# Performance work log

Measured on AMD Instinct MI355X. Metric: run time of the kernel, lower is better.

## Reference

```python
import jax, jax.numpy as jnp
import numpy as np

EPS = 1e-5


def _bn(h, gamma, beta):
    # BatchNorm1d in training mode: batch statistics over node dim
    mu = h.mean(axis=0)
    var = h.var(axis=0)
    return gamma * (h - mu) * jax.lax.rsqrt(var + EPS) + beta


def _rgcn_layer(x, src, dst, etype, W, Wloop, b, n_dst):
    # Relation-specific gather-transform-scatter (DGL RelGraphConv, sum agg,
    # self-loop + bias, no regularizer).
    x_src = x[src]                                   # [E, in] gather
    num_rels = W.shape[0]
    m = jnp.zeros((x_src.shape[0], W.shape[2]), x.dtype)
    for r in range(num_rels):                        # small fixed relation count
        m = m + jnp.where((etype == r)[:, None], x_src @ W[r], 0.0)
    agg = jax.ops.segment_sum(m, dst, num_segments=n_dst)  # scatter-add to dst
    # DGL block convention: dst nodes are the prefix of src nodes
    return agg + x[:n_dst] @ Wloop + b


def setup_inputs() -> dict:
    key = jax.random.key(0)
    ks = jax.random.split(key, 16)
    N_SRC, N_DST0, N_DST1 = 200000, 50000, 10000
    E0, E1, R, H, C = 800000, 160000, 5, 256, 153
    s = 1.0 / np.sqrt(H)
    inp = {
        "x": jax.random.normal(ks[0], (N_SRC, H), jnp.float32),
        "src0": jax.random.randint(ks[1], (E0,), 0, N_SRC, jnp.int32),
        "dst0": jax.random.randint(ks[2], (E0,), 0, N_DST0, jnp.int32),
        "etype0": jax.random.randint(ks[3], (E0,), 0, R, jnp.int32),
        "src1": jax.random.randint(ks[4], (E1,), 0, N_DST0, jnp.int32),
        "dst1": jax.random.randint(ks[5], (E1,), 0, N_DST1, jnp.int32),
        "etype1": jax.random.randint(ks[6], (E1,), 0, R, jnp.int32),
        "n_dst0": N_DST0,
        "n_dst1": N_DST1,
        "W0": jax.random.normal(ks[7], (R, H, H), jnp.float32) * s,
        "Wl0": jax.random.normal(ks[8], (H, H), jnp.float32) * s,
        "b0": jnp.zeros((H,), jnp.float32),
        "g0": jnp.ones((H,), jnp.float32),
        "be0": jnp.zeros((H,), jnp.float32),
        "W1": jax.random.normal(ks[9], (R, H, H), jnp.float32) * s,
        "Wl1": jax.random.normal(ks[10], (H, H), jnp.float32) * s,
        "b1": jnp.zeros((H,), jnp.float32),
        "g1": jnp.ones((H,), jnp.float32),
        "be1": jnp.zeros((H,), jnp.float32),
        "Wm1": jax.random.normal(ks[11], (H, H), jnp.float32) * s,
        "bm1": jnp.zeros((H,), jnp.float32),
        "gm": jnp.ones((H,), jnp.float32),
        "bem": jnp.zeros((H,), jnp.float32),
        "Wm2": jax.random.normal(ks[12], (H, C), jnp.float32) * s,
        "bm2": jnp.zeros((C,), jnp.float32),
    }
    return inp


def reference(x, src0, dst0, etype0, src1, dst1, etype1, n_dst0, n_dst1,
              W0, Wl0, b0, g0, be0, W1, Wl1, b1, g1, be1,
              Wm1, bm1, gm, bem, Wm2, bm2):
    # layer 0
    h = _rgcn_layer(x, src0, dst0, etype0, W0, Wl0, b0, n_dst0)
    h = jax.nn.elu(_bn(h, g0, be0))
    # layer 1
    h = _rgcn_layer(h, src1, dst1, etype1, W1, Wl1, b1, n_dst1)
    h = jax.nn.elu(_bn(h, g1, be1))
    # MLP head (dropout is identity in eval)
    h = jax.nn.relu(_bn(h @ Wm1 + bm1, gm, bem))
    return h @ Wm2 + bm2
```

## Files before the change

kernel.cpp:

```cpp
#include <hip/hip_runtime.h>
#include <hip/hip_bf16.h>


#define HD   256
#define EPS  1e-5f
#define NREL 5
#define ND0  50000
#define ND1  10000

typedef unsigned short ushort_t;
using f32x4  = __attribute__((ext_vector_type(4))) float;
using short8 = __attribute__((ext_vector_type(8))) short;

__device__ __forceinline__ ushort_t f2b(float f) {
    union { float f; unsigned u; } x; x.f = f;
    unsigned r = x.u + 0x7FFF + ((x.u >> 16) & 1);
    return (ushort_t)(r >> 16);
}
__device__ __forceinline__ float b2f(ushort_t h) {
    union { unsigned u; float f; } x; x.u = ((unsigned)h) << 16;
    return x.f;
}

#define GLOAD_LDS16(gp, lp)                                                     \
    __builtin_amdgcn_global_load_lds(                                           \
        (const __attribute__((address_space(1))) unsigned int*)(gp),            \
        (__attribute__((address_space(3))) unsigned int*)(lp), 16, 0, 0)

struct WconvArgs {
    const float* src[14];
    ushort_t*    dst[14];
    int          N[14];
};
__global__ void wconv_all_kernel(WconvArgs a) {
    int mat = blockIdx.x >> 8;
    int id = (blockIdx.x & 255) * 256 + threadIdx.x;
    int n = id >> 8, k = id & 255;
    int N = a.N[mat];
    float v = (n < N) ? a.src[mat][(size_t)k * N + n] : 0.f;
    a.dst[mat][id] = f2b(v);
}

__global__ void xconv_kernel(const float* __restrict__ x, ushort_t* __restrict__ xb,
                             int n4) {
    int id = blockIdx.x * 256 + threadIdx.x;
    if (id >= n4) return;
    float4 v = ((const float4*)x)[id];
    ushort4 o; o.x = f2b(v.x); o.y = f2b(v.y); o.z = f2b(v.z); o.w = f2b(v.w);
    ((ushort4*)xb)[id] = o;
}

__global__ void count2_kernel(const int* __restrict__ d0, const int* __restrict__ e0, int E0,
                              const int* __restrict__ d1, const int* __restrict__ e1, int E1,
                              int* __restrict__ cnt, int* __restrict__ pos) {
    int e = blockIdx.x * 256 + threadIdx.x;
    if (e < E0) {
        pos[e] = atomicAdd(&cnt[e0[e] * ND0 + d0[e]], 1);
    } else if (e < E0 + E1) {
        int i = e - E0;
        pos[e] = atomicAdd(&cnt[NREL * ND0 + e1[i] * ND1 + d1[i]], 1);
    }
}

__global__ void scan_block_kernel(const int* __restrict__ in, int* __restrict__ out,
                                  int* __restrict__ bsum, int nb) {
    __shared__ int ts[256];
    int tid = threadIdx.x;
    int base = blockIdx.x * 1024 + tid * 4;
    int v0 = (base + 0 < nb) ? in[base + 0] : 0;
    int v1 = (base + 1 < nb) ? in[base + 1] : 0;
    int v2 = (base + 2 < nb) ? in[base + 2] : 0;
    int v3 = (base + 3 < nb) ? in[base + 3] : 0;
    int tsum = v0 + v1 + v2 + v3;
    ts[tid] = tsum;
    __syncthreads();
    for (int d = 1; d < 256; d <<= 1) {
        int t = (tid >= d) ? ts[tid - d] : 0;
        __syncthreads();
        ts[tid] += t;
        __syncthreads();
    }
    int excl = ts[tid] - tsum;
    if (base + 0 < nb) out[base + 0] = excl;
    if (base + 1 < nb) out[base + 1] = excl + v0;
    if (base + 2 < nb) out[base + 2] = excl + v0 + v1;
    if (base + 3 < nb) out[base + 3] = excl + v0 + v1 + v2;
    if (tid == 255 && bsum) bsum[blockIdx.x] = ts[255];
}

__global__ void scan_add_kernel(int* __restrict__ out, const int* __restrict__ bsum, int nb) {
    int i = blockIdx.x * 256 + threadIdx.x;
    if (i < nb) out[i] += bsum[i >> 10];
}

__global__ void fill2_kernel(const int* __restrict__ s0, const int* __restrict__ d0,
                             const int* __restrict__ e0, int E0,
                             const int* __restrict__ s1, const int* __restrict__ d1,
                             const int* __restrict__ e1, int E1,
                             const int* __restrict__ pos, const int* __restrict__ off,
                             int* __restrict__ ssrc) {
    int e = blockIdx.x * 256 + threadIdx.x;
    if (e < E0) {
        ssrc[off[e0[e] * ND0 + d0[e]] + pos[e]] = s0[e];
    } else if (e < E0 + E1) {
        int i = e - E0;
        ssrc[off[NREL * ND0 + e1[i] * ND1 + d1[i]] + pos[e]] = s1[i];
    }
}

__global__ void gather_kernel(const ushort_t* __restrict__ feat, const int* __restrict__ ssrc,
                              const int* __restrict__ cnt, const int* __restrict__ off,
                              int nbuckets, ushort_t* __restrict__ out,
                              const float* __restrict__ sc, const float* __restrict__ sh) {
    int wave = (blockIdx.x * 256 + threadIdx.x) >> 6;
    int lane = threadIdx.x & 63;
    if (wave >= nbuckets) return;
    int deg = cnt[wave], s = off[wave];
    float4 scv = {0, 0, 0, 0}, shv = {0, 0, 0, 0};
    if (sc) { scv = ((const float4*)sc)[lane]; shv = ((const float4*)sh)[lane]; }
    float a0 = 0, a1 = 0, a2 = 0, a3 = 0;
    if (sc) {
        for (int j = 0; j < deg; j++) {
            ushort4 v = ((const ushort4*)(feat + (size_t)ssrc[s + j] * HD))[lane];
            float f0 = fmaf(b2f(v.x), scv.x, shv.x);
            float f1 = fmaf(b2f(v.y), scv.y, shv.y);
            float f2 = fmaf(b2f(v.z), scv.z, shv.z);
            float f3 = fmaf(b2f(v.w), scv.w, shv.w);
            a0 += f0 > 0.f ? f0 : expm1f(f0);
            a1 += f1 > 0.f ? f1 : expm1f(f1);
            a2 += f2 > 0.f ? f2 : expm1f(f2);
            a3 += f3 > 0.f ? f3 : expm1f(f3);
        }
    } else {
        int j = 0;
        for (; j + 2 <= deg; j += 2) {
            int r0 = ssrc[s + j], r1 = ssrc[s + j + 1];
            ushort4 v0 = ((const ushort4*)(feat + (size_t)r0 * HD))[lane];
            ushort4 v1 = ((const ushort4*)(feat + (size_t)r1 * HD))[lane];
            a0 += b2f(v0.x) + b2f(v1.x); a1 += b2f(v0.y) + b2f(v1.y);
            a2 += b2f(v0.z) + b2f(v1.z); a3 += b2f(v0.w) + b2f(v1.w);
        }
        if (j < deg) {
            ushort4 v = ((const ushort4*)(feat + (size_t)ssrc[s + j] * HD))[lane];
            a0 += b2f(v.x); a1 += b2f(v.y); a2 += b2f(v.z); a3 += b2f(v.w);
        }
    }
    ushort4 o; o.x = f2b(a0); o.y = f2b(a1); o.z = f2b(a2); o.w = f2b(a3);
    ((ushort4*)(out + (size_t)wave * HD))[lane] = o;
}

__global__ void bnprep_kernel(const float* __restrict__ sums, const float* __restrict__ g,
                              const float* __restrict__ be, float invM,
                              float* __restrict__ sc, float* __restrict__ sh) {
    int c = threadIdx.x;
    float mu = sums[c] * invM;
    float var = sums[HD + c] * invM - mu * mu;
    float s = g[c] * rsqrtf(var + EPS);
    sc[c] = s; sh[c] = be[c] - mu * s;
}

__global__ void bnact_kernel(const ushort_t* __restrict__ in, ushort_t* __restrict__ out,
                             const float* __restrict__ sc, const float* __restrict__ sh,
                             int act, int n64) {
    int id = blockIdx.x * 256 + threadIdx.x;
    if (id >= n64) return;
    int c4 = id & 63;
    ushort4 v = ((const ushort4*)in)[id];
    float4 scv = ((const float4*)sc)[c4];
    float4 shv = ((const float4*)sh)[c4];
    float f0 = fmaf(b2f(v.x), scv.x, shv.x);
    float f1 = fmaf(b2f(v.y), scv.y, shv.y);
    float f2 = fmaf(b2f(v.z), scv.z, shv.z);
    float f3 = fmaf(b2f(v.w), scv.w, shv.w);
    if (act == 2) {
        f0 = fmaxf(f0, 0.f); f1 = fmaxf(f1, 0.f);
        f2 = fmaxf(f2, 0.f); f3 = fmaxf(f3, 0.f);
    } else {
        f0 = f0 > 0.f ? f0 : expm1f(f0);
        f1 = f1 > 0.f ? f1 : expm1f(f1);
        f2 = f2 > 0.f ? f2 : expm1f(f2);
        f3 = f3 > 0.f ? f3 : expm1f(f3);
    }
    ushort4 o; o.x = f2b(f0); o.y = f2b(f1); o.z = f2b(f2); o.w = f2b(f3);
    ((ushort4*)out)[id] = o;
}

struct Seg {
    const ushort_t* A;
    const ushort_t* B;
};
struct GemmArgs {
    Seg seg[6];
    int nseg;
    const float* bias;
    float* stats;
    ushort_t* Cb;
    float* Cf;
    int M, N;
};

__launch_bounds__(256, 2)
__global__ void gemm_ring_kernel(GemmArgs g) {
    __shared__ __align__(1024) ushort_t As[4][4096];
    __shared__ __align__(1024) ushort_t Bs[4][4096];
    int tid = threadIdx.x;
    int w = tid >> 6, lane = tid & 63;
    int rq = lane >> 4, ci = lane & 15;
    int wm = (w >> 1) * 64, wn = (w & 1) * 64;
    int wmf = wm >> 4, wnf = wn >> 4;
    int bm = blockIdx.y * 128, bn = blockIdx.x * 128;
    f32x4 acc[4][4] = {};
    int NT = (g.nseg * HD) >> 5;

    auto stage = [&](int b, int t) {
        int k = t << 5;
        int si = k >> 8, kl = k & 255;
        const ushort_t* Ap = g.seg[si].A;
        const ushort_t* Bp = g.seg[si].B;
        int ft = w * 2;
        GLOAD_LDS16(Ap + (size_t)(bm + ft * 16 + ci) * HD + kl + rq * 8,
                    &As[b][ft * 512 + lane * 8]);
        GLOAD_LDS16(Ap + (size_t)(bm + (ft + 1) * 16 + ci) * HD + kl + rq * 8,
                    &As[b][(ft + 1) * 512 + lane * 8]);
        GLOAD_LDS16(Bp + (size_t)(bn + ft * 16 + ci) * HD + kl + rq * 8,
                    &Bs[b][ft * 512 + lane * 8]);
        GLOAD_LDS16(Bp + (size_t)(bn + (ft + 1) * 16 + ci) * HD + kl + rq * 8,
                    &Bs[b][(ft + 1) * 512 + lane * 8]);
    };

    stage(0, 0);
    if (NT > 1) stage(1, 1);
    if (NT > 2) stage(2, 2);
    for (int t = 0; t < NT; t++) {
        int buf = t & 3;
        int rem = NT - t;
        if (rem >= 3)      asm volatile("s_waitcnt vmcnt(8)" ::: "memory");
        else if (rem == 2) asm volatile("s_waitcnt vmcnt(4)" ::: "memory");
        else               asm volatile("s_waitcnt vmcnt(0)" ::: "memory");
        __builtin_amdgcn_s_barrier();
        __builtin_amdgcn_sched_barrier(0);
        if (t + 3 < NT) stage((t + 3) & 3, t + 3);
        short8 a[4], b[4];
#pragma unroll
        for (int ni = 0; ni < 4; ni++)
            b[ni] = *(const short8*)&Bs[buf][(wnf + ni) * 512 + lane * 8];
#pragma unroll
        for (int mi = 0; mi < 4; mi++)
            a[mi] = *(const short8*)&As[buf][(wmf + mi) * 512 + lane * 8];
#pragma unroll
        for (int mi = 0; mi < 4; mi++)
#pragma unroll
            for (int ni = 0; ni < 4; ni++)
                acc[mi][ni] = __builtin_amdgcn_mfma_f32_16x16x32_bf16(
                    a[mi], b[ni], acc[mi][ni], 0, 0, 0);
    }

#pragma unroll
    for (int ni = 0; ni < 4; ni++) {
        int col = bn + wn + ni * 16 + ci;
        float bv = (col < g.N) ? g.bias[col] : 0.f;
#pragma unroll
        for (int mi = 0; mi < 4; mi++)
#pragma unroll
            for (int reg = 0; reg < 4; reg++) acc[mi][ni][reg] += bv;
    }
    if (g.stats) {
#pragma unroll
        for (int ni = 0; ni < 4; ni++) {
            float s = 0.f, s2 = 0.f;
#pragma unroll
            for (int mi = 0; mi < 4; mi++)
#pragma unroll
                for (int reg = 0; reg < 4; reg++) {
                    int row = bm + wm + mi * 16 + rq * 4 + reg;
                    if (row < g.M) { float v = acc[mi][ni][reg]; s += v; s2 += v * v; }
                }
            s  += __shfl_xor(s, 16);  s  += __shfl_xor(s, 32);
            s2 += __shfl_xor(s2, 16); s2 += __shfl_xor(s2, 32);
            if (rq == 0) {
                int col = bn + wn + ni * 16 + ci;
                atomicAdd(&g.stats[col], s);
                atomicAdd(&g.stats[HD + col], s2);
            }
        }
    }
#pragma unroll
    for (int mi = 0; mi < 4; mi++)
#pragma unroll
        for (int ni = 0; ni < 4; ni++)
#pragma unroll
            for (int reg = 0; reg < 4; reg++) {
                int row = bm + wm + mi * 16 + rq * 4 + reg;
                int col = bn + wn + ni * 16 + ci;
                if (row < g.M && col < g.N) {
                    float v = acc[mi][ni][reg];
                    if (g.Cb) g.Cb[(size_t)row * HD + col] = f2b(v);
                    else      g.Cf[(size_t)row * g.N + col] = v;
                }
            }
}

extern "C" void kernel_launch(void* const* d_in, const int* in_sizes, int n_in,
                              void* d_out, int out_size, void* d_ws, size_t ws_size,
                              hipStream_t stream) {
    const float* x   = (const float*)d_in[0];
    const int* src0  = (const int*)d_in[1];
    const int* dst0  = (const int*)d_in[2];
    const int* et0   = (const int*)d_in[3];
    const int* src1  = (const int*)d_in[4];
    const int* dst1  = (const int*)d_in[5];
    const int* et1   = (const int*)d_in[6];
    const float* W0  = (const float*)d_in[9];
    const float* Wl0 = (const float*)d_in[10];
    const float* b0  = (const float*)d_in[11];
    const float* g0  = (const float*)d_in[12];
    const float* be0 = (const float*)d_in[13];
    const float* W1  = (const float*)d_in[14];
    const float* Wl1 = (const float*)d_in[15];
    const float* b1  = (const float*)d_in[16];
    const float* g1  = (const float*)d_in[17];
    const float* be1 = (const float*)d_in[18];
    const float* Wm1 = (const float*)d_in[19];
    const float* bm1 = (const float*)d_in[20];
    const float* gm  = (const float*)d_in[21];
    const float* bem = (const float*)d_in[22];
    const float* Wm2 = (const float*)d_in[23];
    const float* bm2 = (const float*)d_in[24];

    const int E0 = in_sizes[1];
    const int E1 = in_sizes[4];
    const int NOUT = in_sizes[24];
    const int NSRC = in_sizes[0] / HD;
    const int NBKT = NREL * ND0 + NREL * ND1;

    char* p = (char*)d_ws;
    ushort_t* Wt = (ushort_t*)p;  p += (size_t)14 * 65536 * 2;
    float* st    = (float*)p;     p += 1536 * 4;
    float* bnp   = (float*)p;     p += 6 * 256 * 4;
    int* cnt     = (int*)p;       p += (size_t)NBKT * 4;
    int* off     = (int*)p;       p += (size_t)NBKT * 4;
    int* bsum    = (int*)p;       p += 1024 * 4;
    int* pos     = (int*)p;       p += (size_t)(E0 + E1) * 4;
    int* ssrc    = (int*)p;       p += (size_t)(E0 + E1) * 4;
    ushort_t* xb  = (ushort_t*)p; p += (size_t)NSRC * HD * 2;
    ushort_t* S0  = (ushort_t*)p; p += (size_t)(NREL * ND0 + 512) * HD * 2;
    ushort_t* S1  = (ushort_t*)p; p += (size_t)(NREL * ND1 + 512) * HD * 2;
    ushort_t* h0b = (ushort_t*)p; p += (size_t)(ND0 + 512) * HD * 2;
    ushort_t* h1b = (ushort_t*)p; p += (size_t)(ND1 + 512) * HD * 2;
    ushort_t* mb  = (ushort_t*)p; p += (size_t)(ND1 + 512) * HD * 2;
    ushort_t* h0a = (ushort_t*)p; p += (size_t)(ND1 + 512) * HD * 2;
    ushort_t* h1a = (ushort_t*)p; p += (size_t)(ND1 + 512) * HD * 2;
    ushort_t* ma  = (ushort_t*)p; p += (size_t)(ND1 + 512) * HD * 2;

    float* st0 = st, *st1 = st + 512, *stm = st + 1024;
    float* sc0 = bnp, *sh0 = bnp + 256, *sc1 = bnp + 512, *sh1 = bnp + 768;
    float* scm = bnp + 1024, *shm = bnp + 1280;

    ushort_t* W0t  = Wt;
    ushort_t* Wl0t = Wt + 5 * 65536;
    ushort_t* W1t  = Wt + 6 * 65536;
    ushort_t* Wl1t = Wt + 11 * 65536;
    ushort_t* Wm1t = Wt + 12 * 65536;
    ushort_t* Wm2t = Wt + 13 * 65536;

    {
        WconvArgs wa;
        for (int r = 0; r < NREL; r++) { wa.src[r] = W0 + (size_t)r * 65536; wa.dst[r] = W0t + (size_t)r * 65536; wa.N[r] = 256; }
        wa.src[5] = Wl0; wa.dst[5] = Wl0t; wa.N[5] = 256;
        for (int r = 0; r < NREL; r++) { wa.src[6 + r] = W1 + (size_t)r * 65536; wa.dst[6 + r] = W1t + (size_t)r * 65536; wa.N[6 + r] = 256; }
        wa.src[11] = Wl1; wa.dst[11] = Wl1t; wa.N[11] = 256;
        wa.src[12] = Wm1; wa.dst[12] = Wm1t; wa.N[12] = 256;
        wa.src[13] = Wm2; wa.dst[13] = Wm2t; wa.N[13] = NOUT;
        wconv_all_kernel<<<14 * 256, 256, 0, stream>>>(wa);
    }
    xconv_kernel<<<(NSRC * 64 + 255) / 256, 256, 0, stream>>>(x, xb, NSRC * 64);
    hipMemsetAsync(st, 0, 1536 * sizeof(float), stream);
    hipMemsetAsync(cnt, 0, (size_t)NBKT * sizeof(int), stream);

    int ET = E0 + E1;
    count2_kernel<<<(ET + 255) / 256, 256, 0, stream>>>(dst0, et0, E0, dst1, et1, E1, cnt, pos);
    int nsb = (NBKT + 1023) / 1024;
    scan_block_kernel<<<nsb, 256, 0, stream>>>(cnt, off, bsum, NBKT);
    scan_block_kernel<<<1, 256, 0, stream>>>(bsum, bsum, nullptr, nsb);
    scan_add_kernel<<<(NBKT + 255) / 256, 256, 0, stream>>>(off, bsum, NBKT);
    fill2_kernel<<<(ET + 255) / 256, 256, 0, stream>>>(src0, dst0, et0, E0, src1, dst1, et1, E1, pos, off, ssrc);

    gather_kernel<<<(NREL * ND0 * 64) / 256, 256, 0, stream>>>(
        xb, ssrc, cnt, off, NREL * ND0, S0, nullptr, nullptr);
    {
        GemmArgs ga = {};
        for (int s = 0; s < NREL; s++)
            ga.seg[s] = { S0 + (size_t)s * ND0 * HD, W0t + (size_t)s * 65536 };
        ga.seg[5] = { xb, Wl0t };
        ga.nseg = 6; ga.bias = b0; ga.stats = st0;
        ga.Cb = h0b; ga.Cf = nullptr; ga.M = ND0; ga.N = HD;
        gemm_ring_kernel<<<dim3(2, (ND0 + 127) / 128), 256, 0, stream>>>(ga);
    }
    bnprep_kernel<<<1, 256, 0, stream>>>(st0, g0, be0, 1.f / ND0, sc0, sh0);

    bnact_kernel<<<((ND1 + 512) * 64 + 255) / 256, 256, 0, stream>>>(
        h0b, h0a, sc0, sh0, 1, (ND1 + 512) * 64);
    gather_kernel<<<(NREL * ND1 * 64) / 256, 256, 0, stream>>>(
        h0b, ssrc, cnt + NREL * ND0, off + NREL * ND0, NREL * ND1, S1, sc0, sh0);
    {
        GemmArgs ga = {};
        for (int s = 0; s < NREL; s++)
            ga.seg[s] = { S1 + (size_t)s * ND1 * HD, W1t + (size_t)s * 65536 };
        ga.seg[5] = { h0a, Wl1t };
        ga.nseg = 6; ga.bias = b1; ga.stats = st1;
        ga.Cb = h1b; ga.Cf = nullptr; ga.M = ND1; ga.N = HD;
        gemm_ring_kernel<<<dim3(2, (ND1 + 127) / 128), 256, 0, stream>>>(ga);
    }
    bnprep_kernel<<<1, 256, 0, stream>>>(st1, g1, be1, 1.f / ND1, sc1, sh1);

    bnact_kernel<<<((ND1 + 512) * 64 + 255) / 256, 256, 0, stream>>>(
        h1b, h1a, sc1, sh1, 1, (ND1 + 512) * 64);
    {
        GemmArgs ga = {};
        ga.seg[0] = { h1a, Wm1t };
        ga.nseg = 1; ga.bias = bm1; ga.stats = stm;
        ga.Cb = mb; ga.Cf = nullptr; ga.M = ND1; ga.N = HD;
        gemm_ring_kernel<<<dim3(2, (ND1 + 127) / 128), 256, 0, stream>>>(ga);
    }
    bnprep_kernel<<<1, 256, 0, stream>>>(stm, gm, bem, 1.f / ND1, scm, shm);
    bnact_kernel<<<((ND1 + 512) * 64 + 255) / 256, 256, 0, stream>>>(
        mb, ma, scm, shm, 2, (ND1 + 512) * 64);
    {
        GemmArgs ga = {};
        ga.seg[0] = { ma, Wm2t };
        ga.nseg = 1; ga.bias = bm2; ga.stats = nullptr;
        ga.Cb = nullptr; ga.Cf = (float*)d_out; ga.M = ND1; ga.N = NOUT;
        gemm_ring_kernel<<<dim3((NOUT + 127) / 128, (ND1 + 127) / 128), 256, 0, stream>>>(ga);
    }
}
```

Before: 785.7 us.

## Replace LDS ring-buffered GEMM with register-prefetched direct global loads

The GEMM drops the 4-stage LDS ring (global_load_lds plus barriers) and has each wave load its A/B fragments straight from global memory into registers, keeping three sets in flight. This removes the LDS traffic, the waitcnt/barrier synchronisation and the LDS occupancy cap. In exchange, operand tiles are no longer shared between waves through LDS, so each tile is read from global/L2 memory twice. Register pressure also rises from the three 8-vector sets held alongside the accumulators.

```diff
diff --git a/kernel.cpp b/kernel.cpp
--- a/kernel.cpp
+++ b/kernel.cpp
@@ -21,11 +21,6 @@
     union { unsigned u; float f; } x; x.u = ((unsigned)h) << 16;
     return x.f;
 }
-
-#define GLOAD_LDS16(gp, lp)                                                     \
-    __builtin_amdgcn_global_load_lds(                                           \
-        (const __attribute__((address_space(1))) unsigned int*)(gp),            \
-        (__attribute__((address_space(3))) unsigned int*)(lp), 16, 0, 0)
 
 struct WconvArgs {
     const float* src[14];
@@ -199,60 +194,60 @@
     int M, N;
 };
 
-__launch_bounds__(256, 2)
-__global__ void gemm_ring_kernel(GemmArgs g) {
-    __shared__ __align__(1024) ushort_t As[4][4096];
-    __shared__ __align__(1024) ushort_t Bs[4][4096];
+#define LOADSET(Aset, Bset, t)                                                  \
+    {                                                                           \
+        int si_ = (t) >> 3, kl_ = ((t) & 7) * 32;                               \
+        const ushort_t* Ap_ = g.seg[si_].A + aoff + kl_;                        \
+        const ushort_t* Bp_ = g.seg[si_].B + boff + kl_;                        \
+        Aset[0] = *(const short8*)(Ap_);                                        \
+        Aset[1] = *(const short8*)(Ap_ + 16 * HD);                              \
+        Aset[2] = *(const short8*)(Ap_ + 32 * HD);                              \
+        Aset[3] = *(const short8*)(Ap_ + 48 * HD);                              \
+        Bset[0] = *(const short8*)(Bp_);                                        \
+        Bset[1] = *(const short8*)(Bp_ + 16 * HD);                              \
+        Bset[2] = *(const short8*)(Bp_ + 32 * HD);                              \
+        Bset[3] = *(const short8*)(Bp_ + 48 * HD);                              \
+    }
+
+#define MFMASET(Aset, Bset)                                                     \
+    {                                                                           \
+        _Pragma("unroll")                                                       \
+        for (int mi = 0; mi < 4; mi++)                                          \
+            _Pragma("unroll")                                                   \
+            for (int ni = 0; ni < 4; ni++)                                      \
+                acc[mi][ni] = __builtin_amdgcn_mfma_f32_16x16x32_bf16(          \
+                    Aset[mi], Bset[ni], acc[mi][ni], 0, 0, 0);                  \
+    }
+
+__launch_bounds__(256)
+__global__ void gemm_reg_kernel(GemmArgs g) {
     int tid = threadIdx.x;
     int w = tid >> 6, lane = tid & 63;
     int rq = lane >> 4, ci = lane & 15;
     int wm = (w >> 1) * 64, wn = (w & 1) * 64;
-    int wmf = wm >> 4, wnf = wn >> 4;
     int bm = blockIdx.y * 128, bn = blockIdx.x * 128;
+    size_t aoff = (size_t)(bm + wm + ci) * HD + rq * 8;
+    size_t boff = (size_t)(bn + wn + ci) * HD + rq * 8;
     f32x4 acc[4][4] = {};
-    int NT = (g.nseg * HD) >> 5;
-
-    auto stage = [&](int b, int t) {
-        int k = t << 5;
-        int si = k >> 8, kl = k & 255;
-        const ushort_t* Ap = g.seg[si].A;
-        const ushort_t* Bp = g.seg[si].B;
-        int ft = w * 2;
-        GLOAD_LDS16(Ap + (size_t)(bm + ft * 16 + ci) * HD + kl + rq * 8,
-                    &As[b][ft * 512 + lane * 8]);
-        GLOAD_LDS16(Ap + (size_t)(bm + (ft + 1) * 16 + ci) * HD + kl + rq * 8,
-                    &As[b][(ft + 1) * 512 + lane * 8]);
-        GLOAD_LDS16(Bp + (size_t)(bn + ft * 16 + ci) * HD + kl + rq * 8,
-                    &Bs[b][ft * 512 + lane * 8]);
-        GLOAD_LDS16(Bp + (size_t)(bn + (ft + 1) * 16 + ci) * HD + kl + rq * 8,
-                    &Bs[b][(ft + 1) * 512 + lane * 8]);
-    };
-
-    stage(0, 0);
-    if (NT > 1) stage(1, 1);
-    if (NT > 2) stage(2, 2);
-    for (int t = 0; t < NT; t++) {
-        int buf = t & 3;
-        int rem = NT - t;
-        if (rem >= 3)      asm volatile("s_waitcnt vmcnt(8)" ::: "memory");
-        else if (rem == 2) asm volatile("s_waitcnt vmcnt(4)" ::: "memory");
-        else               asm volatile("s_waitcnt vmcnt(0)" ::: "memory");
-        __builtin_amdgcn_s_barrier();
-        __builtin_amdgcn_sched_barrier(0);
-        if (t + 3 < NT) stage((t + 3) & 3, t + 3);
-        short8 a[4], b[4];
-#pragma unroll
-        for (int ni = 0; ni < 4; ni++)
-            b[ni] = *(const short8*)&Bs[buf][(wnf + ni) * 512 + lane * 8];
-#pragma unroll
-        for (int mi = 0; mi < 4; mi++)
-            a[mi] = *(const short8*)&As[buf][(wmf + mi) * 512 + lane * 8];
-#pragma unroll
-        for (int mi = 0; mi < 4; mi++)
-#pragma unroll
-            for (int ni = 0; ni < 4; ni++)
-                acc[mi][ni] = __builtin_amdgcn_mfma_f32_16x16x32_bf16(
-                    a[mi], b[ni], acc[mi][ni], 0, 0, 0);
+    int NT = g.nseg * 8;
+
+    short8 A0[4], B0[4], A1[4], B1[4], A2[4], B2[4];
+    LOADSET(A0, B0, 0);
+    LOADSET(A1, B1, 1);
+    LOADSET(A2, B2, 2);
+    for (int t = 0; t < NT; t += 3) {
+        {
+            MFMASET(A0, B0);
+            if (t + 3 < NT) LOADSET(A0, B0, t + 3);
+        }
+        if (t + 1 < NT) {
+            MFMASET(A1, B1);
+            if (t + 4 < NT) LOADSET(A1, B1, t + 4);
+        }
+        if (t + 2 < NT) {
+            MFMASET(A2, B2);
+            if (t + 5 < NT) LOADSET(A2, B2, t + 5);
+        }
     }
 
 #pragma unroll
@@ -394,7 +389,7 @@
         ga.seg[5] = { xb, Wl0t };
         ga.nseg = 6; ga.bias = b0; ga.stats = st0;
         ga.Cb = h0b; ga.Cf = nullptr; ga.M = ND0; ga.N = HD;
-        gemm_ring_kernel<<<dim3(2, (ND0 + 127) / 128), 256, 0, stream>>>(ga);
+        gemm_reg_kernel<<<dim3(2, (ND0 + 127) / 128), 256, 0, stream>>>(ga);
     }
     bnprep_kernel<<<1, 256, 0, stream>>>(st0, g0, be0, 1.f / ND0, sc0, sh0);
 
@@ -409,7 +404,7 @@
         ga.seg[5] = { h0a, Wl1t };
         ga.nseg = 6; ga.bias = b1; ga.stats = st1;
         ga.Cb = h1b; ga.Cf = nullptr; ga.M = ND1; ga.N = HD;
-        gemm_ring_kernel<<<dim3(2, (ND1 + 127) / 128), 256, 0, stream>>>(ga);
+        gemm_reg_kernel<<<dim3(2, (ND1 + 127) / 128), 256, 0, stream>>>(ga);
     }
     bnprep_kernel<<<1, 256, 0, stream>>>(st1, g1, be1, 1.f / ND1, sc1, sh1);
 
@@ -420,7 +415,7 @@
         ga.seg[0] = { h1a, Wm1t };
         ga.nseg = 1; ga.bias = bm1; ga.stats = stm;
         ga.Cb = mb; ga.Cf = nullptr; ga.M = ND1; ga.N = HD;
-        gemm_ring_kernel<<<dim3(2, (ND1 + 127) / 128), 256, 0, stream>>>(ga);
+        gemm_reg_kernel<<<dim3(2, (ND1 + 127) / 128), 256, 0, stream>>>(ga);
     }
     bnprep_kernel<<<1, 256, 0, stream>>>(stm, gm, bem, 1.f / ND1, scm, shm);
     bnact_kernel<<<((ND1 + 512) * 64 + 255) / 256, 256, 0, stream>>>(
@@ -430,6 +425,6 @@
         ga.seg[0] = { ma, Wm2t };
         ga.nseg = 1; ga.bias = bm2; ga.stats = nullptr;
         ga.Cb = nullptr; ga.Cf = (float*)d_out; ga.M = ND1; ga.N = NOUT;
-        gemm_ring_kernel<<<dim3((NOUT + 127) / 128, (ND1 + 127) / 128), 256, 0, stream>>>(ga);
-    }
-}
+        gemm_reg_kernel<<<dim3((NOUT + 127) / 128, (ND1 + 127) / 128), 256, 0, stream>>>(ga);
+    }
+}
```

Measured after the change: 841.0 us. 1.07x slower.
